# Performance work log

Measured on AMD Instinct MI355X. Metric: run time of the kernel, lower is better.

## Reference

```python
import jax, jax.numpy as jnp
import numpy as np


def _gru_scan(x, m, d, Wih, Whh, bih, bhh):
    # Returns pre-update hidden at each step (hiddens.append(hidden) BEFORE rnn_cell)
    H = Whh.shape[1]
    B = x.shape[0]
    h0 = jnp.zeros((B, H), x.dtype)
    xs = (jnp.swapaxes(x, 0, 1), jnp.swapaxes(m, 0, 1), jnp.swapaxes(d, 0, 1))  # [T,B,V]

    def step(h, inp):
        xt, mt, dt = inp
        gi = jnp.concatenate([xt, mt, dt], axis=1) @ Wih.T + bih  # [B,3H]
        gh = h @ Whh.T + bhh
        ir, iz, inn = jnp.split(gi, 3, axis=1)
        hr, hz, hn = jnp.split(gh, 3, axis=1)
        r = jax.nn.sigmoid(ir + hr)
        z = jax.nn.sigmoid(iz + hz)
        n = jnp.tanh(inn + r * hn)
        h_new = (1.0 - z) * n + z * h
        return h_new, h

    _, hs = jax.lax.scan(step, h0, xs)
    return jnp.swapaxes(hs, 0, 1)  # [B,T,H]


def setup_inputs() -> dict:
    key = jax.random.key(0)
    B, T, V, H = 512, 128, 59, 512
    ks = jax.random.split(key, 12)

    def u(k, shape, fan_in):
        s = 1.0 / np.sqrt(fan_in).astype(np.float32)
        return jax.random.uniform(k, shape, jnp.float32, -s, s)

    return {
        "values": jax.random.normal(ks[0], (B, T, V), jnp.float32),
        "masks": (jax.random.uniform(ks[1], (B, T, V)) < 0.8).astype(jnp.float32),
        "deltas_f": jax.random.uniform(ks[2], (B, T, V), jnp.float32),
        "deltas_b": jax.random.uniform(ks[3], (B, T, V), jnp.float32),
        # GRUCell(input=3V, hidden=H)
        "Wih": u(ks[4], (3 * H, 3 * V), 3 * V),
        "Whh": u(ks[5], (3 * H, H), H),
        "bih": jnp.zeros((3 * H,), jnp.float32),
        "bhh": jnp.zeros((3 * H,), jnp.float32),
        # hist_reg: Linear(2H -> V)
        "Wh": u(ks[6], (V, 2 * H), 2 * H),
        "bh": jnp.zeros((V,), jnp.float32),
        "Wf": u(ks[7], (V, V), V),
        "bf": jnp.zeros((V,), jnp.float32),
        # weight_combine: Linear(2V -> V)
        "Wc": u(ks[8], (V, 2 * V), 2 * V),
        "bc": jnp.zeros((V,), jnp.float32),
        # imputation: Linear(V -> V)
        "Wi": u(ks[9], (V, V), V),
        "bi": jnp.zeros((V,), jnp.float32),
    }


def reference(values, masks, deltas_f, deltas_b, Wih, Whh, bih, bhh,
              Wh, bh, Wf, bf, Wc, bc, Wi, bi):
    V = values.shape[-1]
    # forward-direction hiddens
    hf = _gru_scan(values, masks, deltas_f, Wih, Whh, bih, bhh)  # [B,T,H]
    # backward-direction: run GRU on time-flipped x/masks with deltas_b, then reverse list
    hb = _gru_scan(values[:, ::-1], masks[:, ::-1], deltas_b, Wih, Whh, bih, bhh)[:, ::-1]
    h = jnp.concatenate([hf, hb], axis=-1)  # [B,T,2H]
    x_v = h @ Wh.T + bh  # hist_reg
    mdiag = 1.0 - jnp.eye(V, dtype=values.dtype)
    x_u = values @ (Wf * mdiag).T + bf  # feat_reg
    x_h = x_u + jnp.concatenate([x_v, masks], axis=-1) @ Wc.T + bc
    imp = x_h @ Wi.T + bi
    # per-timestep masked MAE, summed over T (denominator is per-step mask count)
    num = jnp.sum(jnp.abs(values - imp) * masks, axis=(0, 2))  # [T]
    den = jnp.sum(masks, axis=(0, 2)) + 1e-5
    x_loss = jnp.sum(num / den)
    x_imp = masks * values + (1.0 - masks) * imp
    return x_imp, x_loss
```

## Files before the change

kernel.cpp:

```cpp
#include <hip/hip_runtime.h>
#include <stdint.h>


typedef unsigned short ushort_t;
typedef __bf16 bf16x8 __attribute__((ext_vector_type(8)));
typedef float f32x4 __attribute__((ext_vector_type(4)));
typedef unsigned int u32x4 __attribute__((ext_vector_type(4)));

__device__ __forceinline__ ushort_t f2bf(float f) {
    union { float f; uint32_t u; } c; c.f = f;
    uint32_t u = c.u;
    uint32_t r = (u + 0x7FFFu + ((u >> 16) & 1u)) >> 16;
    return (ushort_t)r;
}

__device__ __forceinline__ u32x4 load_b128_mall(const void* p) {
    u32x4 d;
    asm volatile("global_load_dwordx4 %0, %1, off sc0 sc1"
                 : "=v"(d) : "v"(p) : "memory");
    return d;
}
__device__ __forceinline__ void store_b16_mall(void* p, unsigned v) {
    asm volatile("global_store_short %0, %1, off sc0 sc1"
                 :: "v"(p), "v"(v) : "memory");
}

__device__ __forceinline__ float fast_sigmoid(float x) {
    float e = __expf(-x);
    return __builtin_amdgcn_rcpf(1.f + e);
}
__device__ __forceinline__ float fast_tanh(float x) {
    float xc = fminf(fmaxf(x, -15.f), 15.f);
    float e = __expf(-2.f * xc);
    return (1.f - e) * __builtin_amdgcn_rcpf(1.f + e);
}

__global__ void prep_small(const float* __restrict__ Wih, const float* __restrict__ Whh,
                           const float* __restrict__ Wh,
                           const float* __restrict__ Wf, const float* __restrict__ bf_,
                           const float* __restrict__ Wc, const float* __restrict__ bc,
                           const float* __restrict__ Wi, const float* __restrict__ bi,
                           ushort_t* __restrict__ WhhB, ushort_t* __restrict__ WihB,
                           ushort_t* __restrict__ WhpB,
                           ushort_t* __restrict__ hf0, ushort_t* __restrict__ hb0,
                           float* __restrict__ hstate,
                           ushort_t* __restrict__ Wpost1, ushort_t* __restrict__ Wpost2,
                           float* __restrict__ bcP, float* __restrict__ biP,
                           unsigned* __restrict__ bar)
{
    long long gid = (long long)blockIdx.x * blockDim.x + threadIdx.x;
    long long stride = (long long)gridDim.x * blockDim.x;

    for (long long i = gid; i < 16 * 64; i += stride) bar[i] = 0u;
    for (long long i = gid; i < 1024LL * 512; i += stride) hstate[i] = 0.f;
    for (long long i = gid; i < 512LL * 512; i += stride) { hf0[i] = 0; hb0[i] = 0; }
    for (long long i = gid; i < 1536LL * 512; i += stride) WhhB[i] = f2bf(Whh[i]);
    for (long long i = gid; i < 1536LL * 192; i += stride) {
        int n = (int)(i / 192), c = (int)(i % 192);
        WihB[i] = (c < 177) ? f2bf(Wih[n * 177 + c]) : (ushort_t)0;
    }
    for (long long i = gid; i < 64LL * 1024; i += stride) {
        int n = (int)(i >> 10), k = (int)(i & 1023);
        WhpB[i] = (n < 59) ? f2bf(Wh[n * 1024 + k]) : (ushort_t)0;
    }
    for (long long i = gid; i < 64LL * 192; i += stride) {
        int n = (int)(i / 192), c = (int)(i % 192);
        float w = 0.f;
        if (n < 59) {
            if (c < 59)       w = (c == n) ? 0.f : Wf[n * 59 + c];
            else if (c < 118) w = Wc[n * 118 + (c - 59)];
            else if (c < 177) w = Wc[n * 118 + 59 + (c - 118)];
        }
        Wpost1[i] = f2bf(w);
    }
    for (long long i = gid; i < 64LL * 64; i += stride) {
        int n = (int)(i >> 6), k = (int)(i & 63);
        Wpost2[i] = (n < 59 && k < 59) ? f2bf(Wi[n * 59 + k]) : (ushort_t)0;
    }
    for (long long i = gid; i < 64; i += stride) {
        bcP[i] = (i < 59) ? (bf_[i] + bc[i]) : 0.f;
        biP[i] = (i < 59) ? bi[i] : 0.f;
    }
}

__global__ __launch_bounds__(192)
void prep_panels(const float* __restrict__ values, const float* __restrict__ masks,
                 const float* __restrict__ deltas_f, const float* __restrict__ deltas_b,
                 ushort_t* __restrict__ xcat_f, ushort_t* __restrict__ xcat_b,
                 ushort_t* __restrict__ pcat)
{
    const int row = blockIdx.x;
    const int c = threadIdx.x;
    const int b = row >> 7, t = row & 127;
    const int tr = 127 - t;
    const long long rowr = (long long)b * 128 + tr;

    float vf = 0.f;
    if (c < 59)       vf = values  [(long long)row * 59 + c];
    else if (c < 118) vf = masks   [(long long)row * 59 + (c - 59)];
    else if (c < 177) vf = deltas_f[(long long)row * 59 + (c - 118)];
    xcat_f[((size_t)t * 512 + b) * 192 + c] = (c < 177) ? f2bf(vf) : (ushort_t)0;

    float vb = 0.f;
    if (c < 59)       vb = values  [rowr * 59 + c];
    else if (c < 118) vb = masks   [rowr * 59 + (c - 59)];
    else if (c < 177) vb = deltas_b[(long long)row * 59 + (c - 118)];
    xcat_b[((size_t)t * 512 + b) * 192 + c] = (c < 177) ? f2bf(vb) : (ushort_t)0;

    if (c < 59)
        pcat[(size_t)row * 192 + c] = f2bf(values[(long long)row * 59 + c]);
    else if (c >= 118 && c < 177)
        pcat[(size_t)row * 192 + c] = f2bf(masks[(long long)row * 59 + (c - 118)]);
    else if (c >= 177)
        pcat[(size_t)row * 192 + c] = 0;
}

__global__ __launch_bounds__(512)
void recurrence_kernel(const ushort_t* __restrict__ WhhB, const ushort_t* __restrict__ WihB,
                       const float* __restrict__ bih, const float* __restrict__ bhh,
                       const ushort_t* __restrict__ xcat_f, const ushort_t* __restrict__ xcat_b,
                       ushort_t* __restrict__ hfS, ushort_t* __restrict__ hbS,
                       unsigned* __restrict__ bar)
{
    extern __shared__ char smem_c[];
    ushort_t* Bw = (ushort_t*)smem_c;
    ushort_t* As = Bw + 96 * 704;

    const int tid  = threadIdx.x;
    const int blk  = blockIdx.x;
    const int ublk = blk & 15;
    const int mblk = blk >> 4;
    const int u0   = ublk * 32;
    const bool fwd = (mblk < 8);
    const int rbase = (fwd ? mblk : mblk - 8) * 64;
    const ushort_t* xbase = fwd ? xcat_f : xcat_b;
    ushort_t* hS = fwd ? hfS : hbS;
    unsigned* gctr = bar + (unsigned)mblk * 64;

    for (int i = tid; i < 96 * 88; i += 512) {
        int row = i / 88, q = i - row * 88;
        int g = row >> 5, u = u0 + (row & 31);
        const ushort_t* src = (q < 64)
            ? WhhB + ((size_t)(g * 512 + u)) * 512 + q * 8
            : WihB + ((size_t)(g * 512 + u)) * 192 + (q - 64) * 8;
        int qs = q ^ (row & 7);
        *(u32x4*)&Bw[row * 704 + qs * 8] = *(const u32x4*)src;
    }

    const int lane = tid & 63, wv = tid >> 6;
    const int mt = wv >> 1, tc = wv & 1;
    const int l15 = lane & 15, lhi = lane >> 4;
    const int arow = tid >> 3, aj = tid & 7;
    const int awoff = arow * 64 + ((aj ^ (arow & 7)) * 8);
    const int aSw = l15 & 7;

    const int u = u0 + tc * 16 + l15;
    const float bR  = bih[u] + bhh[u];
    const float bZ  = bih[512 + u] + bhh[512 + u];
    const float bNX = bih[1024 + u];
    const float bNH = bhh[1024 + u];

    f32x4 hreg = {0.f, 0.f, 0.f, 0.f};
    f32x4 zero = {0.f, 0.f, 0.f, 0.f};
    u32x4 r[3];

    {
        const ushort_t* xr0 = xbase + (size_t)(rbase + arow) * 192 + aj * 8;
        r[0] = load_b128_mall(xr0);
        r[1] = load_b128_mall(xr0 + 64);
        r[2] = load_b128_mall(xr0 + 128);
        asm volatile("s_waitcnt vmcnt(0)" ::: "memory");
    }
    __syncthreads();

    for (int t = 0; t < 127; ++t) {
        const ushort_t* hrow = hS + (size_t)t * 262144 + (size_t)(rbase + arow) * 512 + aj * 8;
        ushort_t* hdst = hS + (size_t)(t + 1) * 262144;

        f32x4 accR = zero, accZ = zero, accNH = zero, accNX = zero;

        *(u32x4*)&As[awoff] = r[0];
        __syncthreads();

        #pragma unroll
        for (int c = 0; c < 11; ++c) {
            if (c <= 7) r[c % 3] = load_b128_mall(hrow + c * 64);

            const ushort_t* Ab = As + (c & 1) * 4096;
            #pragma unroll
            for (int ks = 0; ks < 64; ks += 32) {
                int j  = (ks >> 3) + lhi;
                int jB = (c < 3) ? (64 + c * 8 + j) : ((c - 3) * 8 + j);
                bf16x8 a  = *(const bf16x8*)&Ab[(mt * 16 + l15) * 64 + ((j ^ aSw) * 8)];
                bf16x8 b0 = *(const bf16x8*)&Bw[( 0 + tc * 16 + l15) * 704 + ((jB ^ aSw) * 8)];
                bf16x8 b1 = *(const bf16x8*)&Bw[(32 + tc * 16 + l15) * 704 + ((jB ^ aSw) * 8)];
                bf16x8 b2 = *(const bf16x8*)&Bw[(64 + tc * 16 + l15) * 704 + ((jB ^ aSw) * 8)];
                accR = __builtin_amdgcn_mfma_f32_16x16x32_bf16(a, b0, accR, 0, 0, 0);
                accZ = __builtin_amdgcn_mfma_f32_16x16x32_bf16(a, b1, accZ, 0, 0, 0);
                if (c < 3) accNX = __builtin_amdgcn_mfma_f32_16x16x32_bf16(a, b2, accNX, 0, 0, 0);
                else       accNH = __builtin_amdgcn_mfma_f32_16x16x32_bf16(a, b2, accNH, 0, 0, 0);
            }

            if (c < 10) {
                if (c <= 7)      { asm volatile("s_waitcnt vmcnt(2)" ::: "memory"); }
                else if (c == 8) { asm volatile("s_waitcnt vmcnt(1)" ::: "memory"); }
                else             { asm volatile("s_waitcnt vmcnt(0)" ::: "memory"); }
                *(u32x4*)&As[((c + 1) & 1) * 4096 + awoff] = r[(c + 1) % 3];
                __syncthreads();
            }
        }

        #pragma unroll
        for (int reg = 0; reg < 4; ++reg) {
            int m = rbase + mt * 16 + lhi * 4 + reg;
            float rr = fast_sigmoid(accR[reg] + bR);
            float zz = fast_sigmoid(accZ[reg] + bZ);
            float nn = fast_tanh(accNX[reg] + bNX + rr * (accNH[reg] + bNH));
            float hnew = (1.f - zz) * nn + zz * hreg[reg];
            hreg[reg] = hnew;
            store_b16_mall(hdst + (size_t)m * 512 + u, (unsigned)f2bf(hnew));
        }

        if (t < 126) {
            const ushort_t* xrn = xbase + (size_t)(t + 1) * 98304
                                + (size_t)(rbase + arow) * 192 + aj * 8;
            r[0] = load_b128_mall(xrn);
            r[1] = load_b128_mall(xrn + 64);
            r[2] = load_b128_mall(xrn + 128);

            asm volatile("s_waitcnt vmcnt(0)" ::: "memory");
            __syncthreads();
            if (tid == 0) {
                atomicAdd(gctr, 1u);
                unsigned target = (unsigned)(t + 1) * 16u;
                while (__hip_atomic_load(gctr, __ATOMIC_RELAXED,
                                         __HIP_MEMORY_SCOPE_AGENT) < target)
                    __builtin_amdgcn_s_sleep(1);
            }
            __syncthreads();
        }
    }
}

__global__ __launch_bounds__(512)
void step_kernel(const ushort_t* __restrict__ hsrcF, const ushort_t* __restrict__ hsrcB,
                 ushort_t* __restrict__ hdstF, ushort_t* __restrict__ hdstB,
                 const ushort_t* __restrict__ xF, const ushort_t* __restrict__ xB,
                 const ushort_t* __restrict__ WhhB, const ushort_t* __restrict__ WihB,
                 const float* __restrict__ bih, const float* __restrict__ bhh,
                 float* __restrict__ hstate)
{
    __shared__ __align__(16) ushort_t As[64 * 64];
    __shared__ __align__(16) ushort_t Bs[96 * 64];

    const int tid  = threadIdx.x;
    const int ublk = blockIdx.x;
    const int mblk = blockIdx.y;
    const int u0   = ublk * 32;
    const bool fwd = (mblk < 8);
    const ushort_t* hsrc = fwd ? hsrcF : hsrcB;
    const ushort_t* xsrc = fwd ? xF : xB;
    ushort_t* hdst = fwd ? hdstF : hdstB;
    const int rbase = (fwd ? mblk : mblk - 8) * 64;

    const int lane = tid & 63, wv = tid >> 6;
    const int mt = wv >> 1, tc = wv & 1;
    const int l15 = lane & 15, lhi = lane >> 4;

    f32x4 zero = {0.f, 0.f, 0.f, 0.f};
    f32x4 accR = zero, accZ = zero, accNH = zero, accNX = zero;
    const int arow = tid >> 3, ac8 = (tid & 7) * 8;

    for (int chunk = 0; chunk < 11; ++chunk) {
        const bool ph1 = (chunk < 8);
        {
            const ushort_t* src = ph1
                ? hsrc + ((size_t)(rbase + arow)) * 512 + chunk * 64 + ac8
                : xsrc + ((size_t)(rbase + arow)) * 192 + (chunk - 8) * 64 + ac8;
            *(uint4*)&As[arow * 64 + ac8] = *(const uint4*)src;
        }
        {
            int rowB = tid >> 3; int c8 = (tid & 7) * 8;
            int g = rowB >> 5; int u = u0 + (rowB & 31);
            const ushort_t* src = ph1
                ? WhhB + ((size_t)(g * 512 + u)) * 512 + chunk * 64 + c8
                : WihB + ((size_t)(g * 512 + u)) * 192 + (chunk - 8) * 64 + c8;
            *(uint4*)&Bs[rowB * 64 + c8] = *(const uint4*)src;
            if (tid < 256) {
                int u2 = tid + 512;
                rowB = u2 >> 3; c8 = (u2 & 7) * 8;
                g = rowB >> 5; u = u0 + (rowB & 31);
                src = ph1
                    ? WhhB + ((size_t)(g * 512 + u)) * 512 + chunk * 64 + c8
                    : WihB + ((size_t)(g * 512 + u)) * 192 + (chunk - 8) * 64 + c8;
                *(uint4*)&Bs[rowB * 64 + c8] = *(const uint4*)src;
            }
        }
        __syncthreads();
        #pragma unroll
        for (int ks = 0; ks < 64; ks += 32) {
            bf16x8 a  = *(const bf16x8*)&As[(mt * 16 + l15) * 64 + ks + lhi * 8];
            bf16x8 b0 = *(const bf16x8*)&Bs[( 0 + tc * 16 + l15) * 64 + ks + lhi * 8];
            bf16x8 b1 = *(const bf16x8*)&Bs[(32 + tc * 16 + l15) * 64 + ks + lhi * 8];
            bf16x8 b2 = *(const bf16x8*)&Bs[(64 + tc * 16 + l15) * 64 + ks + lhi * 8];
            accR = __builtin_amdgcn_mfma_f32_16x16x32_bf16(a, b0, accR, 0, 0, 0);
            accZ = __builtin_amdgcn_mfma_f32_16x16x32_bf16(a, b1, accZ, 0, 0, 0);
            if (ph1) accNH = __builtin_amdgcn_mfma_f32_16x16x32_bf16(a, b2, accNH, 0, 0, 0);
            else     accNX = __builtin_amdgcn_mfma_f32_16x16x32_bf16(a, b2, accNX, 0, 0, 0);
        }
        __syncthreads();
    }

    const int u = u0 + tc * 16 + l15;
    const float bR  = bih[u] + bhh[u];
    const float bZ  = bih[512 + u] + bhh[512 + u];
    const float bNX = bih[1024 + u];
    const float bNH = bhh[1024 + u];
    #pragma unroll
    for (int reg = 0; reg < 4; ++reg) {
        int m = mblk * 64 + mt * 16 + lhi * 4 + reg;
        float r = 1.f / (1.f + __expf(-(accR[reg] + bR)));
        float z = 1.f / (1.f + __expf(-(accZ[reg] + bZ)));
        float n = tanhf(accNX[reg] + bNX + r * (accNH[reg] + bNH));
        size_t idx = (size_t)m * 512 + u;
        float hold = hstate[idx];
        float hnew = (1.f - z) * n + z * hold;
        hstate[idx] = hnew;
        size_t bloc = (size_t)(fwd ? m : m - 512) * 512 + u;
        hdst[bloc] = f2bf(hnew);
    }
}

__global__ __launch_bounds__(256)
void xv_kernel(const ushort_t* __restrict__ hf, const ushort_t* __restrict__ hb,
               const ushort_t* __restrict__ WhpB, const float* __restrict__ bh,
               ushort_t* __restrict__ pcat)
{
    __shared__ __align__(16) ushort_t As[128 * 64];
    __shared__ __align__(16) ushort_t Bs[64 * 64];
    const int b = blockIdx.x;
    const int tid = threadIdx.x;
    const int lane = tid & 63, wv = tid >> 6;
    const int l15 = lane & 15, lhi = lane >> 4;

    f32x4 zero = {0.f, 0.f, 0.f, 0.f};
    f32x4 acc[2][4];
    #pragma unroll
    for (int i = 0; i < 2; ++i)
        #pragma unroll
        for (int j = 0; j < 4; ++j) acc[i][j] = zero;

    for (int chunk = 0; chunk < 16; ++chunk) {
        const bool fw = (chunk < 8);
        #pragma unroll
        for (int s = 0; s < 4; ++s) {
            int unit = tid + s * 256;
            int row = unit >> 3;
            int c8 = (unit & 7) * 8;
            const ushort_t* src = fw
                ? hf + ((size_t)row * 512 + b) * 512 + chunk * 64 + c8
                : hb + ((size_t)(127 - row) * 512 + b) * 512 + (chunk - 8) * 64 + c8;
            *(uint4*)&As[row * 64 + c8] = *(const uint4*)src;
        }
        #pragma unroll
        for (int s = 0; s < 2; ++s) {
            int unit = tid + s * 256;
            int row = unit >> 3;
            int c8 = (unit & 7) * 8;
            *(uint4*)&Bs[row * 64 + c8] =
                *(const uint4*)(WhpB + (size_t)row * 1024 + chunk * 64 + c8);
        }
        __syncthreads();
        #pragma unroll
        for (int ks = 0; ks < 64; ks += 32) {
            bf16x8 bfr[4];
            #pragma unroll
            for (int nt = 0; nt < 4; ++nt)
                bfr[nt] = *(const bf16x8*)&Bs[(nt * 16 + l15) * 64 + ks + lhi * 8];
            #pragma unroll
            for (int mt2 = 0; mt2 < 2; ++mt2) {
                bf16x8 a = *(const bf16x8*)&As[(wv * 32 + mt2 * 16 + l15) * 64 + ks + lhi * 8];
                #pragma unroll
                for (int nt = 0; nt < 4; ++nt)
                    acc[mt2][nt] = __builtin_amdgcn_mfma_f32_16x16x32_bf16(a, bfr[nt], acc[mt2][nt], 0, 0, 0);
            }
        }
        __syncthreads();
    }
    #pragma unroll
    for (int mt2 = 0; mt2 < 2; ++mt2) {
        #pragma unroll
        for (int nt = 0; nt < 4; ++nt) {
            int col = nt * 16 + l15;
            if (col < 59) {
                float bhc = bh[col];
                #pragma unroll
                for (int reg = 0; reg < 4; ++reg) {
                    int t = wv * 32 + mt2 * 16 + lhi * 4 + reg;
                    pcat[((size_t)b * 128 + t) * 192 + 59 + col] = f2bf(acc[mt2][nt][reg] + bhc);
                }
            }
        }
    }
}

__global__ __launch_bounds__(256)
void post_kernel(const ushort_t* __restrict__ pcat,
                 const ushort_t* __restrict__ Wpost1, const ushort_t* __restrict__ Wpost2,
                 const float* __restrict__ bcP, const float* __restrict__ biP,
                 const float* __restrict__ values, const float* __restrict__ masks,
                 float* __restrict__ out, float* __restrict__ pnum, float* __restrict__ pden)
{
    __shared__ __align__(16) ushort_t A1[64 * 200];
    __shared__ __align__(16) ushort_t B1[64 * 200];
    __shared__ __align__(16) ushort_t B2[64 * 72];

    const int tid = threadIdx.x;
    const int blk = blockIdx.x;
    const int lane = tid & 63, wv = tid >> 6;
    const int l15 = lane & 15, lhi = lane >> 4;

    #pragma unroll
    for (int s = 0; s < 6; ++s) {
        int unit = tid + s * 256;
        int row = unit / 24, c8 = (unit % 24) * 8;
        *(uint4*)&A1[row * 200 + c8] =
            *(const uint4*)(pcat + ((size_t)blk * 64 + row) * 192 + c8);
        *(uint4*)&B1[row * 200 + c8] =
            *(const uint4*)(Wpost1 + (size_t)row * 192 + c8);
    }
    #pragma unroll
    for (int s = 0; s < 2; ++s) {
        int unit = tid + s * 256;
        int row = unit >> 3, c8 = (unit & 7) * 8;
        *(uint4*)&B2[row * 72 + c8] = *(const uint4*)(Wpost2 + (size_t)row * 64 + c8);
    }
    __syncthreads();

    f32x4 zero = {0.f, 0.f, 0.f, 0.f};
    f32x4 acc1[4];
    #pragma unroll
    for (int nt = 0; nt < 4; ++nt) acc1[nt] = zero;

    #pragma unroll
    for (int ks = 0; ks < 192; ks += 32) {
        bf16x8 a = *(const bf16x8*)&A1[(wv * 16 + l15) * 200 + ks + lhi * 8];
        #pragma unroll
        for (int nt = 0; nt < 4; ++nt) {
            bf16x8 bb = *(const bf16x8*)&B1[(nt * 16 + l15) * 200 + ks + lhi * 8];
            acc1[nt] = __builtin_amdgcn_mfma_f32_16x16x32_bf16(a, bb, acc1[nt], 0, 0, 0);
        }
    }
    __syncthreads();

    #pragma unroll
    for (int nt = 0; nt < 4; ++nt) {
        int col = nt * 16 + l15;
        float bcv = bcP[col];
        #pragma unroll
        for (int reg = 0; reg < 4; ++reg) {
            int row = wv * 16 + lhi * 4 + reg;
            A1[row * 72 + col] = f2bf(acc1[nt][reg] + bcv);
        }
    }
    __syncthreads();

    f32x4 acc2[4];
    #pragma unroll
    for (int nt = 0; nt < 4; ++nt) acc2[nt] = zero;
    #pragma unroll
    for (int ks = 0; ks < 64; ks += 32) {
        bf16x8 a = *(const bf16x8*)&A1[(wv * 16 + l15) * 72 + ks + lhi * 8];
        #pragma unroll
        for (int nt = 0; nt < 4; ++nt) {
            bf16x8 bb = *(const bf16x8*)&B2[(nt * 16 + l15) * 72 + ks + lhi * 8];
            acc2[nt] = __builtin_amdgcn_mfma_f32_16x16x32_bf16(a, bb, acc2[nt], 0, 0, 0);
        }
    }

    float biR[4];
    #pragma unroll
    for (int nt = 0; nt < 4; ++nt) biR[nt] = biP[nt * 16 + l15];

    #pragma unroll
    for (int reg = 0; reg < 4; ++reg) {
        size_t rowg = (size_t)blk * 64 + wv * 16 + lhi * 4 + reg;
        float esum = 0.f, dsum = 0.f;
        #pragma unroll
        for (int nt = 0; nt < 4; ++nt) {
            int col = nt * 16 + l15;
            if (col < 59) {
                float imp = acc2[nt][reg] + biR[nt];
                float v = values[rowg * 59 + col];
                float m = masks [rowg * 59 + col];
                out[rowg * 59 + col] = m * v + (1.f - m) * imp;
                esum += fabsf(v - imp) * m;
                dsum += m;
            }
        }
        #pragma unroll
        for (int o = 1; o < 16; o <<= 1) {
            esum += __shfl_xor(esum, o);
            dsum += __shfl_xor(dsum, o);
        }
        if (l15 == 0) { pnum[rowg] = esum; pden[rowg] = dsum; }
    }
}

__global__ __launch_bounds__(512)
void loss_kernel(const float* __restrict__ pnum, const float* __restrict__ pden,
                 float* __restrict__ out)
{
    __shared__ float sn[512], sd[512];
    int tid = threadIdx.x;
    int t = tid & 127, q = tid >> 7;
    float a = 0.f, b = 0.f;
    for (int i = 0; i < 128; ++i) {
        int bb = q * 128 + i;
        a += pnum[(size_t)bb * 128 + t];
        b += pden[(size_t)bb * 128 + t];
    }
    sn[tid] = a; sd[tid] = b;
    __syncthreads();
    if (q == 0) {
        float A = sn[t] + sn[128 + t] + sn[256 + t] + sn[384 + t];
        float B = sd[t] + sd[128 + t] + sd[256 + t] + sd[384 + t];
        sn[t] = A / (B + 1e-5f);
    }
    __syncthreads();
    if (tid == 0) {
        float s = 0.f;
        for (int i = 0; i < 128; ++i) s += sn[i];
        out[3866624] = s;
    }
}

extern "C" void kernel_launch(void* const* d_in, const int* in_sizes, int n_in,
                              void* d_out, int out_size, void* d_ws, size_t ws_size,
                              hipStream_t stream)
{
    const float* values   = (const float*)d_in[0];
    const float* masks    = (const float*)d_in[1];
    const float* deltas_f = (const float*)d_in[2];
    const float* deltas_b = (const float*)d_in[3];
    const float* Wih = (const float*)d_in[4];
    const float* Whh = (const float*)d_in[5];
    const float* bih = (const float*)d_in[6];
    const float* bhh = (const float*)d_in[7];
    const float* Wh  = (const float*)d_in[8];
    const float* bh  = (const float*)d_in[9];
    const float* Wf  = (const float*)d_in[10];
    const float* bf_ = (const float*)d_in[11];
    const float* Wc  = (const float*)d_in[12];
    const float* bc  = (const float*)d_in[13];
    const float* Wi  = (const float*)d_in[14];
    const float* bi  = (const float*)d_in[15];
    float* out = (float*)d_out;

    uint8_t* ws = (uint8_t*)d_ws;
    size_t off = 0;
    auto alloc = [&](size_t bytes) -> void* {
        void* p = ws + off;
        off = (off + bytes + 255) & ~((size_t)255);
        return p;
    };
    ushort_t* xcat_f = (ushort_t*)alloc(128ULL * 512 * 192 * 2);
    ushort_t* xcat_b = (ushort_t*)alloc(128ULL * 512 * 192 * 2);
    ushort_t* WhhB   = (ushort_t*)alloc(1536ULL * 512 * 2);
    ushort_t* WihB   = (ushort_t*)alloc(1536ULL * 192 * 2);
    ushort_t* WhpB   = (ushort_t*)alloc(64ULL * 1024 * 2);
    ushort_t* hfS    = (ushort_t*)alloc(128ULL * 512 * 512 * 2);
    ushort_t* hbS    = (ushort_t*)alloc(128ULL * 512 * 512 * 2);
    float*    hstate = (float*)alloc(1024ULL * 512 * 4);
    ushort_t* pcat   = (ushort_t*)alloc(65536ULL * 192 * 2);
    ushort_t* Wpost1 = (ushort_t*)alloc(64ULL * 192 * 2);
    ushort_t* Wpost2 = (ushort_t*)alloc(64ULL * 64 * 2);
    float*    bcP    = (float*)alloc(64 * 4);
    float*    biP    = (float*)alloc(64 * 4);
    float*    pnum   = (float*)alloc(65536ULL * 4);
    float*    pden   = (float*)alloc(65536ULL * 4);
    unsigned* bar    = (unsigned*)alloc(16 * 64 * 4);

    prep_small<<<1024, 256, 0, stream>>>(Wih, Whh, Wh, Wf, bf_, Wc, bc, Wi, bi,
                                         WhhB, WihB, WhpB, hfS, hbS, hstate,
                                         Wpost1, Wpost2, bcP, biP, bar);
    prep_panels<<<65536, 192, 0, stream>>>(values, masks, deltas_f, deltas_b,
                                           xcat_f, xcat_b, pcat);

    const unsigned smemBytes = (96u * 704u + 2u * 64u * 64u) * 2u;
    hipError_t aerr = hipFuncSetAttribute((const void*)recurrence_kernel,
                                          hipFuncAttributeMaxDynamicSharedMemorySize,
                                          (int)smemBytes);
    hipError_t lerr = hipErrorUnknown;
    if (aerr == hipSuccess) {
        const ushort_t* a0 = WhhB; const ushort_t* a1 = WihB;
        const float* a2 = bih; const float* a3 = bhh;
        const ushort_t* a4 = xcat_f; const ushort_t* a5 = xcat_b;
        ushort_t* a6 = hfS; ushort_t* a7 = hbS;
        unsigned* a8 = bar;
        void* args[] = { &a0, &a1, &a2, &a3, &a4, &a5, &a6, &a7, &a8 };
        lerr = hipLaunchCooperativeKernel((const void*)recurrence_kernel,
                                          dim3(256), dim3(512), args, smemBytes, stream);
    }
    if (lerr != hipSuccess) {
        for (int t = 0; t < 127; ++t) {
            step_kernel<<<dim3(16, 16), 512, 0, stream>>>(
                hfS + (size_t)t * 512 * 512, hbS + (size_t)t * 512 * 512,
                hfS + (size_t)(t + 1) * 512 * 512, hbS + (size_t)(t + 1) * 512 * 512,
                xcat_f + (size_t)t * 512 * 192, xcat_b + (size_t)t * 512 * 192,
                WhhB, WihB, bih, bhh, hstate);
        }
    }

    xv_kernel<<<512, 256, 0, stream>>>(hfS, hbS, WhpB, bh, pcat);
    post_kernel<<<1024, 256, 0, stream>>>(pcat, Wpost1, Wpost2, bcP, biP,
                                          values, masks, out, pnum, pden);
    loss_kernel<<<1, 512, 0, stream>>>(pnum, pden, out);
}
```

Baseline: 843.9 us.

## Overlap x-projection MFMAs with hidden-state fetch in persistent GRU loop

```diff
diff --git a/kernel.cpp b/kernel.cpp
--- a/kernel.cpp
+++ b/kernel.cpp
@@ -14,15 +14,18 @@
     return (ushort_t)r;
 }
 
+__device__ __forceinline__ u32x4 load_b128_cached(const void* p) {
+    u32x4 d;
+    asm volatile("global_load_dwordx4 %0, %1, off" : "=v"(d) : "v"(p) : "memory");
+    return d;
+}
 __device__ __forceinline__ u32x4 load_b128_mall(const void* p) {
     u32x4 d;
-    asm volatile("global_load_dwordx4 %0, %1, off sc0 sc1"
-                 : "=v"(d) : "v"(p) : "memory");
+    asm volatile("global_load_dwordx4 %0, %1, off sc0 sc1" : "=v"(d) : "v"(p) : "memory");
     return d;
 }
 __device__ __forceinline__ void store_b16_mall(void* p, unsigned v) {
-    asm volatile("global_store_short %0, %1, off sc0 sc1"
-                 :: "v"(p), "v"(v) : "memory");
+    asm volatile("global_store_short %0, %1, off sc0 sc1" :: "v"(p), "v"(v) : "memory");
 }
 
 __device__ __forceinline__ float fast_sigmoid(float x) {
@@ -159,57 +162,78 @@
     const float bZ  = bih[512 + u] + bhh[512 + u];
     const float bNX = bih[1024 + u];
     const float bNH = bhh[1024 + u];
+    asm volatile("" :: "v"(bR), "v"(bZ), "v"(bNX), "v"(bNH));
+    asm volatile("s_waitcnt vmcnt(0) lgkmcnt(0)" ::: "memory");
+    __syncthreads();
 
     f32x4 hreg = {0.f, 0.f, 0.f, 0.f};
     f32x4 zero = {0.f, 0.f, 0.f, 0.f};
-    u32x4 r[3];
+    u32x4 rx[3];
+    u32x4 rh[8];
+    f32x4 accR = zero, accZ = zero, accNX = zero, accNH = zero;
+
+    auto mfma_pos = [&](int cbuf, int jBbase, f32x4& accN) {
+        const ushort_t* Ab = As + cbuf * 4096;
+        #pragma unroll
+        for (int ks = 0; ks < 64; ks += 32) {
+            int j  = (ks >> 3) + lhi;
+            int jB = jBbase + j;
+            bf16x8 a  = *(const bf16x8*)&Ab[(mt * 16 + l15) * 64 + ((j ^ aSw) * 8)];
+            bf16x8 b0 = *(const bf16x8*)&Bw[( 0 + tc * 16 + l15) * 704 + ((jB ^ aSw) * 8)];
+            bf16x8 b1 = *(const bf16x8*)&Bw[(32 + tc * 16 + l15) * 704 + ((jB ^ aSw) * 8)];
+            bf16x8 b2 = *(const bf16x8*)&Bw[(64 + tc * 16 + l15) * 704 + ((jB ^ aSw) * 8)];
+            accR = __builtin_amdgcn_mfma_f32_16x16x32_bf16(a, b0, accR, 0, 0, 0);
+            accZ = __builtin_amdgcn_mfma_f32_16x16x32_bf16(a, b1, accZ, 0, 0, 0);
+            accN = __builtin_amdgcn_mfma_f32_16x16x32_bf16(a, b2, accN, 0, 0, 0);
+        }
+    };
 
     {
         const ushort_t* xr0 = xbase + (size_t)(rbase + arow) * 192 + aj * 8;
-        r[0] = load_b128_mall(xr0);
-        r[1] = load_b128_mall(xr0 + 64);
-        r[2] = load_b128_mall(xr0 + 128);
-        asm volatile("s_waitcnt vmcnt(0)" ::: "memory");
-    }
+        rx[0] = load_b128_cached(xr0);
+        rx[1] = load_b128_cached(xr0 + 64);
+        rx[2] = load_b128_cached(xr0 + 128);
+    }
+    asm volatile("s_waitcnt vmcnt(0)" ::: "memory");
+
+    {
+        const ushort_t* hrow = hS + (size_t)(rbase + arow) * 512 + aj * 8;
+        #pragma unroll
+        for (int j = 0; j < 8; ++j) rh[j] = load_b128_mall(hrow + j * 64);
+    }
+
+    *(u32x4*)&As[4096 + awoff] = rx[0]; __syncthreads();
+    mfma_pos(1, 64, accNX);
+    *(u32x4*)&As[awoff] = rx[1]; __syncthreads();
+    mfma_pos(0, 72, accNX);
+    *(u32x4*)&As[4096 + awoff] = rx[2]; __syncthreads();
+    mfma_pos(1, 80, accNX);
+
+#define S2_STAGE(JN, WN)                                                      \
+    asm volatile("s_waitcnt vmcnt(" #WN ")" ::: "memory");                    \
+    *(u32x4*)&As[((JN) & 1) * 4096 + awoff] = rh[JN];                         \
     __syncthreads();
 
     for (int t = 0; t < 127; ++t) {
-        const ushort_t* hrow = hS + (size_t)t * 262144 + (size_t)(rbase + arow) * 512 + aj * 8;
+        {
+            const ushort_t* xrn = xbase + (size_t)(t + 1) * 98304
+                                + (size_t)(rbase + arow) * 192 + aj * 8;
+            rx[0] = load_b128_cached(xrn);
+            rx[1] = load_b128_cached(xrn + 64);
+            rx[2] = load_b128_cached(xrn + 128);
+        }
+
+        accNH = zero;
+        S2_STAGE(0, 10) mfma_pos(0,  0, accNH);
+        S2_STAGE(1,  9) mfma_pos(1,  8, accNH);
+        S2_STAGE(2,  8) mfma_pos(0, 16, accNH);
+        S2_STAGE(3,  7) mfma_pos(1, 24, accNH);
+        S2_STAGE(4,  6) mfma_pos(0, 32, accNH);
+        S2_STAGE(5,  5) mfma_pos(1, 40, accNH);
+        S2_STAGE(6,  4) mfma_pos(0, 48, accNH);
+        S2_STAGE(7,  3) mfma_pos(1, 56, accNH);
+
         ushort_t* hdst = hS + (size_t)(t + 1) * 262144;
-
-        f32x4 accR = zero, accZ = zero, accNH = zero, accNX = zero;
-
-        *(u32x4*)&As[awoff] = r[0];
-        __syncthreads();
-
-        #pragma unroll
-        for (int c = 0; c < 11; ++c) {
-            if (c <= 7) r[c % 3] = load_b128_mall(hrow + c * 64);
-
-            const ushort_t* Ab = As + (c & 1) * 4096;
-            #pragma unroll
-            for (int ks = 0; ks < 64; ks += 32) {
-                int j  = (ks >> 3) + lhi;
-                int jB = (c < 3) ? (64 + c * 8 + j) : ((c - 3) * 8 + j);
-                bf16x8 a  = *(const bf16x8*)&Ab[(mt * 16 + l15) * 64 + ((j ^ aSw) * 8)];
-                bf16x8 b0 = *(const bf16x8*)&Bw[( 0 + tc * 16 + l15) * 704 + ((jB ^ aSw) * 8)];
-                bf16x8 b1 = *(const bf16x8*)&Bw[(32 + tc * 16 + l15) * 704 + ((jB ^ aSw) * 8)];
-                bf16x8 b2 = *(const bf16x8*)&Bw[(64 + tc * 16 + l15) * 704 + ((jB ^ aSw) * 8)];
-                accR = __builtin_amdgcn_mfma_f32_16x16x32_bf16(a, b0, accR, 0, 0, 0);
-                accZ = __builtin_amdgcn_mfma_f32_16x16x32_bf16(a, b1, accZ, 0, 0, 0);
-                if (c < 3) accNX = __builtin_amdgcn_mfma_f32_16x16x32_bf16(a, b2, accNX, 0, 0, 0);
-                else       accNH = __builtin_amdgcn_mfma_f32_16x16x32_bf16(a, b2, accNH, 0, 0, 0);
-            }
-
-            if (c < 10) {
-                if (c <= 7)      { asm volatile("s_waitcnt vmcnt(2)" ::: "memory"); }
-                else if (c == 8) { asm volatile("s_waitcnt vmcnt(1)" ::: "memory"); }
-                else             { asm volatile("s_waitcnt vmcnt(0)" ::: "memory"); }
-                *(u32x4*)&As[((c + 1) & 1) * 4096 + awoff] = r[(c + 1) % 3];
-                __syncthreads();
-            }
-        }
-
         #pragma unroll
         for (int reg = 0; reg < 4; ++reg) {
             int m = rbase + mt * 16 + lhi * 4 + reg;
@@ -220,16 +244,10 @@
             hreg[reg] = hnew;
             store_b16_mall(hdst + (size_t)m * 512 + u, (unsigned)f2bf(hnew));
         }
+        asm volatile("s_waitcnt vmcnt(0)" ::: "memory");
+        __syncthreads();
 
         if (t < 126) {
-            const ushort_t* xrn = xbase + (size_t)(t + 1) * 98304
-                                + (size_t)(rbase + arow) * 192 + aj * 8;
-            r[0] = load_b128_mall(xrn);
-            r[1] = load_b128_mall(xrn + 64);
-            r[2] = load_b128_mall(xrn + 128);
-
-            asm volatile("s_waitcnt vmcnt(0)" ::: "memory");
-            __syncthreads();
             if (tid == 0) {
                 atomicAdd(gctr, 1u);
                 unsigned target = (unsigned)(t + 1) * 16u;
@@ -238,8 +256,24 @@
                     __builtin_amdgcn_s_sleep(1);
             }
             __syncthreads();
-        }
-    }
+
+            {
+                const ushort_t* hrow = hS + (size_t)(t + 1) * 262144
+                                     + (size_t)(rbase + arow) * 512 + aj * 8;
+                #pragma unroll
+                for (int j = 0; j < 8; ++j) rh[j] = load_b128_mall(hrow + j * 64);
+            }
+
+            accR = zero; accZ = zero; accNX = zero;
+            *(u32x4*)&As[4096 + awoff] = rx[0]; __syncthreads();
+            mfma_pos(1, 64, accNX);
+            *(u32x4*)&As[awoff] = rx[1]; __syncthreads();
+            mfma_pos(0, 72, accNX);
+            *(u32x4*)&As[4096 + awoff] = rx[2]; __syncthreads();
+            mfma_pos(1, 80, accNX);
+        }
+    }
+#undef S2_STAGE
 }
 
 __global__ __launch_bounds__(512)
```

Measured after the change: 877.0 us. +3.9%, slower.
